# Kernel optimization log

Hardware: AMD Instinct MI355X
Metric: run time of the kernel (lower is better)

The kernel has to match this reference:

```python
import jax, jax.numpy as jnp
import numpy as np

DIM = 1536      # model dim
NH = 12         # num heads
HD = 128        # head dim
F, H, W = 3, 26, 48   # video latent grid (frames, height, width)
S = F * H * W   # sequence length = 3744
B = 1
EPS = 1e-6
C2 = HD // 2    # 64 rotary pairs per head
SPLITS = [C2 - 2 * (C2 // 3), C2 // 3, C2 // 3]  # [22, 21, 21] for (f, h, w)


def _rope_angles():
    """Wan rope_params: concat of per-axis inverse-frequency angle tables, [1024, 64]."""
    def rp(dim):  # returns [1024, dim//2]
        inv = 1.0 / (10000.0 ** (np.arange(0, dim, 2, dtype=np.float64) / dim))
        return np.outer(np.arange(1024, dtype=np.float64), inv)
    a = np.concatenate([rp(HD - 4 * (HD // 6)), rp(2 * (HD // 6)), rp(2 * (HD // 6))], axis=1)
    return jnp.asarray(a, jnp.float32)


def setup_inputs() -> dict:
    key = jax.random.key(0)
    ks = jax.random.split(key, 9)
    std = DIM ** -0.5
    return {
        "x": jax.random.normal(ks[0], (B, S, DIM), jnp.float32),
        "wq": jax.random.normal(ks[1], (DIM, DIM), jnp.float32) * std,
        "bq": jnp.zeros((DIM,), jnp.float32),
        "wk": jax.random.normal(ks[2], (DIM, DIM), jnp.float32) * std,
        "bk": jnp.zeros((DIM,), jnp.float32),
        "wv": jax.random.normal(ks[3], (DIM, DIM), jnp.float32) * std,
        "bv": jnp.zeros((DIM,), jnp.float32),
        "wo": jax.random.normal(ks[4], (DIM, DIM), jnp.float32) * std,
        "bo": jnp.zeros((DIM,), jnp.float32),
        "gq": jnp.ones((DIM,), jnp.float32),   # WanRMSNorm weight for q
        "gk": jnp.ones((DIM,), jnp.float32),   # WanRMSNorm weight for k
        "freqs": _rope_angles(),                # [1024, 64] rotary angles
        "seq_lens": jnp.full((B,), S, jnp.int32),
    }


def _rmsnorm(y, g):
    return y * jax.lax.rsqrt(jnp.mean(jnp.square(y), axis=-1, keepdims=True) + EPS) * g


def _rope_grid(freqs):
    """Build per-position rotary angles [S, C2] from the 3D grid (F,H,W)."""
    af = freqs[:F, :SPLITS[0]]                       # [F, 22]
    ah = freqs[:H, SPLITS[0]:SPLITS[0] + SPLITS[1]]  # [H, 21]
    aw = freqs[:W, SPLITS[0] + SPLITS[1]:]           # [W, 21]
    ang = jnp.concatenate([
        jnp.broadcast_to(af[:, None, None, :], (F, H, W, SPLITS[0])),
        jnp.broadcast_to(ah[None, :, None, :], (F, H, W, SPLITS[1])),
        jnp.broadcast_to(aw[None, None, :, :], (F, H, W, SPLITS[2])),
    ], axis=-1)
    return ang.reshape(S, C2)


def _rope_apply(t, cos, sin):
    # t: [B, S, NH, HD]; pairs (even, odd) rotated by angle.
    tp = t.reshape(B, S, NH, C2, 2)
    xr, xi = tp[..., 0], tp[..., 1]
    yr = xr * cos - xi * sin
    yi = xr * sin + xi * cos
    return jnp.stack([yr, yi], axis=-1).reshape(B, S, NH, HD)


def reference(x, wq, bq, wk, bk, wv, bv, wo, bo, gq, gk, freqs, seq_lens):
    q = _rmsnorm(x @ wq.T + bq, gq).reshape(B, S, NH, HD)
    k = _rmsnorm(x @ wk.T + bk, gk).reshape(B, S, NH, HD)
    v = (x @ wv.T + bv).reshape(B, S, NH, HD)

    ang = _rope_grid(freqs)                    # [S, C2]
    cos = jnp.cos(ang)[None, :, None, :]       # [1, S, 1, C2]
    sin = jnp.sin(ang)[None, :, None, :]
    q = _rope_apply(q, cos, sin)
    k = _rope_apply(k, cos, sin)

    scale = HD ** -0.5
    scores = jnp.einsum('bqhd,bkhd->bhqk', q, k) * scale   # [B, NH, S, S]
    kmask = jnp.arange(S)[None, :] < seq_lens[:, None]     # [B, S]
    scores = jnp.where(kmask[:, None, None, :], scores, jnp.float32(-1e9))
    attn = jax.nn.softmax(scores, axis=-1)
    out = jnp.einsum('bhqk,bkhd->bqhd', attn, v).reshape(B, S, DIM)
    return out @ wo.T + bo
```

## Files before the change

### kernel.cpp

```cpp
#include <hip/hip_runtime.h>
#include <stdint.h>


#define DIM   1536
#define S_TOT 3744
#define NHEAD 12
#define HD    128

using short8 = __attribute__((ext_vector_type(8))) short;
using f32x4  = __attribute__((ext_vector_type(4))) float;
using f32x2  = __attribute__((ext_vector_type(2))) float;

__device__ __forceinline__ unsigned short f2bf(float f) {
  unsigned u = __builtin_bit_cast(unsigned, f);
  u += 0x7fffu + ((u >> 16) & 1u);
  return (unsigned short)(u >> 16);
}

__device__ __forceinline__ void gl_lds16(const void* g, void* l) {
  auto gp = (const __attribute__((address_space(1))) unsigned int*)g;
  auto lp = (__attribute__((address_space(3))) unsigned int*)(uintptr_t)l;
  __builtin_amdgcn_global_load_lds(gp, lp, 16, 0, 0);
}

#define NX4 (S_TOT * DIM / 4)
#define NW4 (DIM * DIM / 4)
__global__ __launch_bounds__(256) void cvt5_kernel(
    const float* __restrict__ x, const float* __restrict__ wq,
    const float* __restrict__ wk, const float* __restrict__ wv,
    const float* __restrict__ wo,
    unsigned short* __restrict__ xb, unsigned short* __restrict__ wqb,
    unsigned short* __restrict__ wkb, unsigned short* __restrict__ wvb,
    unsigned short* __restrict__ wob) {
  int gid = blockIdx.x * 256 + threadIdx.x;
  const float* src; unsigned short* dst; int off;
  if (gid < NX4)                { src = x;  dst = xb;  off = gid; }
  else if (gid < NX4 + NW4)     { src = wq; dst = wqb; off = gid - NX4; }
  else if (gid < NX4 + 2 * NW4) { src = wk; dst = wkb; off = gid - NX4 - NW4; }
  else if (gid < NX4 + 3 * NW4) { src = wv; dst = wvb; off = gid - NX4 - 2 * NW4; }
  else if (gid < NX4 + 4 * NW4) { src = wo; dst = wob; off = gid - NX4 - 3 * NW4; }
  else return;
  float4 v = ((const float4*)src)[off];
  ushort4 o;
  o.x = f2bf(v.x); o.y = f2bf(v.y); o.z = f2bf(v.z); o.w = f2bf(v.w);
  ((ushort4*)dst)[off] = o;
}

__device__ __forceinline__ void gemm_body(const unsigned short* __restrict__ A,
                                          const unsigned short* __restrict__ W,
                                          const float* __restrict__ bias,
                                          float* __restrict__ outF,
                                          unsigned short* __restrict__ outB,
                                          int M, int mode) {
  constexpr int K = DIM, N = DIM;
  __shared__ unsigned short As[128 * 32];
  __shared__ unsigned short Ws[128 * 32];
  int tid = threadIdx.x;
  int w = tid >> 6, lane = tid & 63;
  int wr = w >> 1, wc = w & 1, q4 = lane >> 4, ql = lane & 15;
  int m0 = blockIdx.y * 128, n0 = blockIdx.x * 128;

  f32x4 acc[4][4];
  const f32x4 zero4 = {0.f, 0.f, 0.f, 0.f};
#pragma unroll
  for (int i = 0; i < 4; i++)
#pragma unroll
    for (int j = 0; j < 4; j++) acc[i][j] = zero4;

  for (int k0 = 0; k0 < K; k0 += 32) {
    __syncthreads();
#pragma unroll
    for (int r = 0; r < 2; r++) {
      int idx = r * 256 + tid;
      int row = idx >> 2, ch = idx & 3;
      int am = m0 + row; am = (am < M) ? am : (M - 1);
      gl_lds16(A + (size_t)am * K + k0 + ch * 8, &As[idx * 8]);
      gl_lds16(W + (size_t)(n0 + row) * K + k0 + ch * 8, &Ws[idx * 8]);
    }
    __syncthreads();
    short8 af[4], wf[4];
#pragma unroll
    for (int i = 0; i < 4; i++)
      af[i] = *(const short8*)&As[(wr * 64 + i * 16 + ql) * 32 + q4 * 8];
#pragma unroll
    for (int j = 0; j < 4; j++)
      wf[j] = *(const short8*)&Ws[(wc * 64 + j * 16 + ql) * 32 + q4 * 8];
#pragma unroll
    for (int i = 0; i < 4; i++)
#pragma unroll
      for (int j = 0; j < 4; j++)
        acc[i][j] = __builtin_amdgcn_mfma_f32_16x16x32_bf16(af[i], wf[j], acc[i][j], 0, 0, 0);
  }

  float bb[4];
#pragma unroll
  for (int j = 0; j < 4; j++) bb[j] = bias[n0 + wc * 64 + j * 16 + ql];
#pragma unroll
  for (int i = 0; i < 4; i++) {
#pragma unroll
    for (int rg = 0; rg < 4; rg++) {
      int row = m0 + wr * 64 + i * 16 + q4 * 4 + rg;
      if (row < M) {
#pragma unroll
        for (int j = 0; j < 4; j++) {
          int col = n0 + wc * 64 + j * 16 + ql;
          float v = acc[i][j][rg] + bb[j];
          if (mode == 0) outF[(size_t)row * N + col] = v;
          else           outB[(size_t)row * N + col] = f2bf(v);
        }
      }
    }
  }
}

__global__ __launch_bounds__(256) void gemm_qkv_kernel(
    const unsigned short* __restrict__ xb,
    const unsigned short* __restrict__ wqb, const unsigned short* __restrict__ wkb,
    const unsigned short* __restrict__ wvb,
    const float* __restrict__ bq, const float* __restrict__ bk, const float* __restrict__ bv,
    float* __restrict__ Yq, float* __restrict__ Yk, unsigned short* __restrict__ Vb) {
  int z = blockIdx.z;
  const unsigned short* W = (z == 0) ? wqb : ((z == 1) ? wkb : wvb);
  const float* bias       = (z == 0) ? bq  : ((z == 1) ? bk  : bv);
  float* outF             = (z == 0) ? Yq  : Yk;
  gemm_body(xb, W, bias, outF, Vb, S_TOT, (z == 2) ? 1 : 0);
}

__global__ __launch_bounds__(256) void gemm_out_kernel(
    const unsigned short* __restrict__ AO, const unsigned short* __restrict__ wob,
    const float* __restrict__ bo, float* __restrict__ out) {
  gemm_body(AO, wob, bo, out, nullptr, S_TOT, 0);
}

__global__ __launch_bounds__(256) void normrope_kernel(
    const float* __restrict__ Yq, const float* __restrict__ Yk,
    const float* __restrict__ gq, const float* __restrict__ gk,
    const float* __restrict__ freqs,
    unsigned short* __restrict__ Qb, unsigned short* __restrict__ Kb) {
  int s = blockIdx.x;
  int tid = threadIdx.x;
  int w = tid >> 6, lane = tid & 63;
  const f32x2* yq2 = (const f32x2*)(Yq + (size_t)s * DIM);
  const f32x2* yk2 = (const f32x2*)(Yk + (size_t)s * DIM);
  f32x2 vq[3], vk[3];
  float ssq = 0.f, ssk = 0.f;
#pragma unroll
  for (int r = 0; r < 3; r++) {
    int p = tid + 256 * r;
    vq[r] = yq2[p]; vk[r] = yk2[p];
    ssq += vq[r].x * vq[r].x + vq[r].y * vq[r].y;
    ssk += vk[r].x * vk[r].x + vk[r].y * vk[r].y;
  }
#pragma unroll
  for (int d = 1; d < 64; d <<= 1) {
    ssq += __shfl_xor(ssq, d);
    ssk += __shfl_xor(ssk, d);
  }
  __shared__ float rq[4], rk[4];
  if (lane == 0) { rq[w] = ssq; rk[w] = ssk; }
  __syncthreads();
  float tq = rq[0] + rq[1] + rq[2] + rq[3];
  float tk = rk[0] + rk[1] + rk[2] + rk[3];
  float invq = rsqrtf(tq * (1.f / DIM) + 1e-6f);
  float invk = rsqrtf(tk * (1.f / DIM) + 1e-6f);

  int fi = s / (26 * 48);
  int hi = (s / 48) % 26;
  int wi = s % 48;
#pragma unroll
  for (int r = 0; r < 3; r++) {
    int p = tid + 256 * r;
    int c = p & 63;
    int frow = (c < 22) ? fi : ((c < 43) ? hi : wi);
    float ang = freqs[frow * 64 + c];
    float sn, cs;
    __sincosf(ang, &sn, &cs);
    {
      float a = vq[r].x * invq * gq[2 * p];
      float b = vq[r].y * invq * gq[2 * p + 1];
      ushort2 o; o.x = f2bf(a * cs - b * sn); o.y = f2bf(a * sn + b * cs);
      ((ushort2*)Qb)[(size_t)s * (DIM / 2) + p] = o;
    }
    {
      float a = vk[r].x * invk * gk[2 * p];
      float b = vk[r].y * invk * gk[2 * p + 1];
      ushort2 o; o.x = f2bf(a * cs - b * sn); o.y = f2bf(a * sn + b * cs);
      ((ushort2*)Kb)[(size_t)s * (DIM / 2) + p] = o;
    }
  }
}

__global__ __launch_bounds__(256) void vtrans_kernel(const unsigned short* __restrict__ Vb,
                                                     unsigned short* __restrict__ Vt) {
  int d0 = blockIdx.x * 64, s0 = blockIdx.y * 64;
  __shared__ unsigned short t[64][65];
  int tid = threadIdx.x;
#pragma unroll
  for (int r = 0; r < 4; r++) {
    int idx = r * 256 + tid;
    int sr = idx >> 4, c4 = (idx & 15) * 4;
    ushort4 v; v.x = v.y = v.z = v.w = 0;
    int s = s0 + sr;
    if (s < S_TOT) v = *(const ushort4*)(Vb + (size_t)s * DIM + d0 + c4);
    t[sr][c4 + 0] = v.x; t[sr][c4 + 1] = v.y; t[sr][c4 + 2] = v.z; t[sr][c4 + 3] = v.w;
  }
  __syncthreads();
#pragma unroll
  for (int r = 0; r < 4; r++) {
    int idx = r * 256 + tid;
    int dr = idx >> 4, s4 = (idx & 15) * 4;
    if (s0 + s4 < S_TOT) {
      ushort4 v;
      v.x = t[s4 + 0][dr]; v.y = t[s4 + 1][dr]; v.z = t[s4 + 2][dr]; v.w = t[s4 + 3][dr];
      *(ushort4*)(Vt + (size_t)(d0 + dr) * S_TOT + s0 + s4) = v;
    }
  }
}

__global__ __launch_bounds__(128, 2) void attn_kernel(
    const unsigned short* __restrict__ Qb, const unsigned short* __restrict__ Kb,
    const unsigned short* __restrict__ Vt, unsigned short* __restrict__ AO,
    const int* __restrict__ seq_lens) {
  int h = blockIdx.y;
  int tid = threadIdx.x;
  int w = tid >> 6, lane = tid & 63;
  int q4 = lane >> 4, ql = lane & 15;
  int seqlen = seq_lens[0]; if (seqlen > S_TOT) seqlen = S_TOT;

  __shared__ unsigned short Kl[64 * 128];
  __shared__ unsigned short Vl[128 * 64];
  __shared__ unsigned short Pl[2][32 * 72];
  __shared__ float stat[2][32];

  int q0 = blockIdx.x * 64 + w * 32;
  bool wact = (q0 < S_TOT);

  short8 qf[2][4];
#pragma unroll
  for (int qh = 0; qh < 2; qh++) {
    int qrow = q0 + qh * 16 + ql; if (qrow > S_TOT - 1) qrow = S_TOT - 1;
#pragma unroll
    for (int ks = 0; ks < 4; ks++)
      qf[qh][ks] = *(const short8*)(Qb + (size_t)qrow * DIM + h * HD + ks * 32 + q4 * 8);
  }

  f32x4 o[2][8];
  const f32x4 zero4 = {0.f, 0.f, 0.f, 0.f};
#pragma unroll
  for (int qh = 0; qh < 2; qh++)
#pragma unroll
    for (int nt = 0; nt < 8; nt++) o[qh][nt] = zero4;
  float m_run[2] = {-3.0e38f, -3.0e38f}, l_run[2] = {0.f, 0.f};
  const float sm_scale = 0.08838834764831845f;

  const size_t hoff = (size_t)h * HD;

  for (int kt = 0; kt < (S_TOT + 63) / 64; kt++) {
    int k0 = kt * 64;
    __syncthreads();
    {
      const unsigned short* kseg = Kb + (size_t)k0 * DIM + hoff;
#pragma unroll
      for (int r = 0; r < 8; r++) {
        int idx = r * 128 + tid;
        int row = idx >> 4, c = idx & 15;
        int g = c ^ (row & 15);
        gl_lds16(kseg + (size_t)row * DIM + g * 8, &Kl[idx * 8]);
      }
      int kmax = S_TOT - 8 - k0;
#pragma unroll
      for (int r = 0; r < 8; r++) {
        int idx = r * 128 + tid;
        int row = idx >> 3, c = idx & 7;
        int g = c ^ (row & 7);
        int kc = g * 8; if (kc > kmax) kc = kmax;
        gl_lds16(Vt + (hoff + row) * S_TOT + k0 + kc, &Vl[idx * 8]);
      }
    }
    __syncthreads();
    if (!wact) continue;

    f32x4 st[4][2];
#pragma unroll
    for (int mt = 0; mt < 4; mt++) {
      st[mt][0] = zero4; st[mt][1] = zero4;
#pragma unroll
      for (int ks = 0; ks < 4; ks++) {
        int c = (ks * 4 + q4) ^ ql;
        short8 kf = *(const short8*)&Kl[(mt * 16 + ql) * 128 + c * 8];
        st[mt][0] = __builtin_amdgcn_mfma_f32_16x16x32_bf16(kf, qf[0][ks], st[mt][0], 0, 0, 0);
        st[mt][1] = __builtin_amdgcn_mfma_f32_16x16x32_bf16(kf, qf[1][ks], st[mt][1], 0, 0, 0);
      }
    }

#pragma unroll
    for (int qh = 0; qh < 2; qh++) {
      float sc[16];
      float mloc = -3.0e38f;
#pragma unroll
      for (int mt = 0; mt < 4; mt++)
#pragma unroll
        for (int rg = 0; rg < 4; rg++) {
          int key = k0 + mt * 16 + q4 * 4 + rg;
          float v = st[mt][qh][rg] * sm_scale;
          v = (key < seqlen) ? v : -3.0e38f;
          sc[mt * 4 + rg] = v;
          mloc = fmaxf(mloc, v);
        }
      mloc = fmaxf(mloc, __shfl_xor(mloc, 16));
      mloc = fmaxf(mloc, __shfl_xor(mloc, 32));
      float mnew = fmaxf(m_run[qh], mloc);
      float alpha = __expf(m_run[qh] - mnew);
      m_run[qh] = mnew;
      float lloc = 0.f;
#pragma unroll
      for (int mt = 0; mt < 4; mt++) {
        ushort4 pk;
        float p0 = (k0 + mt * 16 + q4 * 4 + 0 < seqlen) ? __expf(sc[mt * 4 + 0] - mnew) : 0.f;
        float p1 = (k0 + mt * 16 + q4 * 4 + 1 < seqlen) ? __expf(sc[mt * 4 + 1] - mnew) : 0.f;
        float p2 = (k0 + mt * 16 + q4 * 4 + 2 < seqlen) ? __expf(sc[mt * 4 + 2] - mnew) : 0.f;
        float p3 = (k0 + mt * 16 + q4 * 4 + 3 < seqlen) ? __expf(sc[mt * 4 + 3] - mnew) : 0.f;
        lloc += p0 + p1 + p2 + p3;
        pk.x = f2bf(p0); pk.y = f2bf(p1); pk.z = f2bf(p2); pk.w = f2bf(p3);
        *(ushort4*)&Pl[w][(qh * 16 + ql) * 72 + mt * 16 + q4 * 4] = pk;
      }
      lloc += __shfl_xor(lloc, 16);
      lloc += __shfl_xor(lloc, 32);
      l_run[qh] = l_run[qh] * alpha + lloc;
      if (lane < 16) stat[w][qh * 16 + lane] = alpha;
    }

    float ar[2][4];
#pragma unroll
    for (int qh = 0; qh < 2; qh++)
#pragma unroll
      for (int rg = 0; rg < 4; rg++) ar[qh][rg] = stat[w][qh * 16 + q4 * 4 + rg];
#pragma unroll
    for (int qh = 0; qh < 2; qh++)
#pragma unroll
      for (int nt = 0; nt < 8; nt++)
#pragma unroll
        for (int rg = 0; rg < 4; rg++) o[qh][nt][rg] *= ar[qh][rg];

#pragma unroll
    for (int ks2 = 0; ks2 < 2; ks2++) {
      short8 pa0 = *(const short8*)&Pl[w][(0 * 16 + ql) * 72 + ks2 * 32 + q4 * 8];
      short8 pa1 = *(const short8*)&Pl[w][(1 * 16 + ql) * 72 + ks2 * 32 + q4 * 8];
#pragma unroll
      for (int nt = 0; nt < 8; nt++) {
        int c = (ks2 * 4 + q4) ^ (ql & 7);
        short8 vb = *(const short8*)&Vl[(nt * 16 + ql) * 64 + c * 8];
        o[0][nt] = __builtin_amdgcn_mfma_f32_16x16x32_bf16(pa0, vb, o[0][nt], 0, 0, 0);
        o[1][nt] = __builtin_amdgcn_mfma_f32_16x16x32_bf16(pa1, vb, o[1][nt], 0, 0, 0);
      }
    }
  }

  if (wact) {
    if (lane < 16) {
      stat[w][lane]      = 1.0f / l_run[0];
      stat[w][16 + lane] = 1.0f / l_run[1];
    }
#pragma unroll
    for (int qh = 0; qh < 2; qh++) {
#pragma unroll
      for (int rg = 0; rg < 4; rg++) {
        int row = q0 + qh * 16 + q4 * 4 + rg;
        if (row < S_TOT) {
          float il = stat[w][qh * 16 + q4 * 4 + rg];
#pragma unroll
          for (int nt = 0; nt < 8; nt++)
            AO[(size_t)row * DIM + h * HD + nt * 16 + ql] = f2bf(o[qh][nt][rg] * il);
        }
      }
    }
  }
}

extern "C" void kernel_launch(void* const* d_in, const int* in_sizes, int n_in,
                              void* d_out, int out_size, void* d_ws, size_t ws_size,
                              hipStream_t stream) {
  const float* x    = (const float*)d_in[0];
  const float* wq   = (const float*)d_in[1];
  const float* bq   = (const float*)d_in[2];
  const float* wk   = (const float*)d_in[3];
  const float* bk   = (const float*)d_in[4];
  const float* wv   = (const float*)d_in[5];
  const float* bv   = (const float*)d_in[6];
  const float* wo   = (const float*)d_in[7];
  const float* bo   = (const float*)d_in[8];
  const float* gq   = (const float*)d_in[9];
  const float* gk   = (const float*)d_in[10];
  const float* freqs = (const float*)d_in[11];
  const int*   seq  = (const int*)d_in[12];

  char* ws = (char*)d_ws;
  const size_t SZ_X = (size_t)S_TOT * DIM * 2;
  const size_t SZ_W = (size_t)DIM * DIM * 2;
  const size_t SZ_Y = (size_t)S_TOT * DIM * 4;

  unsigned short* xb  = (unsigned short*)(ws);
  unsigned short* wqb = (unsigned short*)(ws + SZ_X);
  unsigned short* wkb = (unsigned short*)(ws + SZ_X + SZ_W);
  unsigned short* wvb = (unsigned short*)(ws + SZ_X + 2 * SZ_W);
  unsigned short* wob = (unsigned short*)(ws + SZ_X + 3 * SZ_W);
  float*          Yq  = (float*)(ws + SZ_X + 4 * SZ_W);
  float*          Yk  = (float*)(ws + SZ_X + 4 * SZ_W + SZ_Y);
  unsigned short* Vb  = (unsigned short*)(ws + SZ_X + 4 * SZ_W + 2 * SZ_Y);
  unsigned short* Qb  = (unsigned short*)(ws + SZ_X + 4 * SZ_W + 2 * SZ_Y + SZ_X);
  unsigned short* Kb  = (unsigned short*)(ws + SZ_X + 4 * SZ_W + 2 * SZ_Y + 2 * SZ_X);
  unsigned short* Vt  = (unsigned short*)(ws + SZ_X + 4 * SZ_W + 2 * SZ_Y + 3 * SZ_X);
  unsigned short* AO  = (unsigned short*)(ws + SZ_X + 4 * SZ_W + 2 * SZ_Y + 4 * SZ_X);

  int total4 = NX4 + 4 * NW4;
  cvt5_kernel<<<dim3((total4 + 255) / 256), 256, 0, stream>>>(
      x, wq, wk, wv, wo, xb, wqb, wkb, wvb, wob);

  gemm_qkv_kernel<<<dim3(DIM / 128, (S_TOT + 127) / 128, 3), 256, 0, stream>>>(
      xb, wqb, wkb, wvb, bq, bk, bv, Yq, Yk, Vb);

  normrope_kernel<<<dim3(S_TOT), 256, 0, stream>>>(Yq, Yk, gq, gk, freqs, Qb, Kb);

  vtrans_kernel<<<dim3(DIM / 64, (S_TOT + 63) / 64), 256, 0, stream>>>(Vb, Vt);

  attn_kernel<<<dim3((S_TOT + 63) / 64, NHEAD), 128, 0, stream>>>(Qb, Kb, Vt, AO, seq);

  gemm_out_kernel<<<dim3(DIM / 128, (S_TOT + 127) / 128), 256, 0, stream>>>(
      AO, wob, bo, (float*)d_out);
}
```

Measured before the change: 473.9 us.

## Split attention into four 16-row waves with lazy rescale and exp2 softmax

```diff
diff --git a/kernel.cpp b/kernel.cpp
--- a/kernel.cpp
+++ b/kernel.cpp
@@ -217,7 +217,7 @@
   }
 }
 
-__global__ __launch_bounds__(128, 2) void attn_kernel(
+__global__ __launch_bounds__(256, 3) void attn_kernel(
     const unsigned short* __restrict__ Qb, const unsigned short* __restrict__ Kb,
     const unsigned short* __restrict__ Vt, unsigned short* __restrict__ AO,
     const int* __restrict__ seq_lens) {
@@ -229,29 +229,25 @@
 
   __shared__ unsigned short Kl[64 * 128];
   __shared__ unsigned short Vl[128 * 64];
-  __shared__ unsigned short Pl[2][32 * 72];
-  __shared__ float stat[2][32];
-
-  int q0 = blockIdx.x * 64 + w * 32;
+  __shared__ unsigned short Pl[4][16 * 72];
+
+  int q0 = blockIdx.x * 64 + w * 16;
   bool wact = (q0 < S_TOT);
 
-  short8 qf[2][4];
-#pragma unroll
-  for (int qh = 0; qh < 2; qh++) {
-    int qrow = q0 + qh * 16 + ql; if (qrow > S_TOT - 1) qrow = S_TOT - 1;
+  short8 qf[4];
+  {
+    int qrow = q0 + ql; if (qrow > S_TOT - 1) qrow = S_TOT - 1;
 #pragma unroll
     for (int ks = 0; ks < 4; ks++)
-      qf[qh][ks] = *(const short8*)(Qb + (size_t)qrow * DIM + h * HD + ks * 32 + q4 * 8);
-  }
-
-  f32x4 o[2][8];
+      qf[ks] = *(const short8*)(Qb + (size_t)qrow * DIM + h * HD + ks * 32 + q4 * 8);
+  }
+
+  f32x4 o[8];
   const f32x4 zero4 = {0.f, 0.f, 0.f, 0.f};
 #pragma unroll
-  for (int qh = 0; qh < 2; qh++)
-#pragma unroll
-    for (int nt = 0; nt < 8; nt++) o[qh][nt] = zero4;
-  float m_run[2] = {-3.0e38f, -3.0e38f}, l_run[2] = {0.f, 0.f};
-  const float sm_scale = 0.08838834764831845f;
+  for (int nt = 0; nt < 8; nt++) o[nt] = zero4;
+  float m_run = -3.0e38f, l_run = 0.f;
+  const float sm_l2 = 0.08838834764831845f * 1.4426950408889634f;
 
   const size_t hoff = (size_t)h * HD;
 
@@ -261,16 +257,16 @@
     {
       const unsigned short* kseg = Kb + (size_t)k0 * DIM + hoff;
 #pragma unroll
-      for (int r = 0; r < 8; r++) {
-        int idx = r * 128 + tid;
+      for (int r = 0; r < 4; r++) {
+        int idx = r * 256 + tid;
         int row = idx >> 4, c = idx & 15;
         int g = c ^ (row & 15);
         gl_lds16(kseg + (size_t)row * DIM + g * 8, &Kl[idx * 8]);
       }
       int kmax = S_TOT - 8 - k0;
 #pragma unroll
-      for (int r = 0; r < 8; r++) {
-        int idx = r * 128 + tid;
+      for (int r = 0; r < 4; r++) {
+        int idx = r * 256 + tid;
         int row = idx >> 3, c = idx & 7;
         int g = c ^ (row & 7);
         int kc = g * 8; if (kc > kmax) kc = kmax;
@@ -280,98 +276,93 @@
     __syncthreads();
     if (!wact) continue;
 
-    f32x4 st[4][2];
+    f32x4 st[4];
 #pragma unroll
     for (int mt = 0; mt < 4; mt++) {
-      st[mt][0] = zero4; st[mt][1] = zero4;
+      st[mt] = zero4;
 #pragma unroll
       for (int ks = 0; ks < 4; ks++) {
         int c = (ks * 4 + q4) ^ ql;
         short8 kf = *(const short8*)&Kl[(mt * 16 + ql) * 128 + c * 8];
-        st[mt][0] = __builtin_amdgcn_mfma_f32_16x16x32_bf16(kf, qf[0][ks], st[mt][0], 0, 0, 0);
-        st[mt][1] = __builtin_amdgcn_mfma_f32_16x16x32_bf16(kf, qf[1][ks], st[mt][1], 0, 0, 0);
-      }
-    }
-
-#pragma unroll
-    for (int qh = 0; qh < 2; qh++) {
-      float sc[16];
-      float mloc = -3.0e38f;
+        st[mt] = __builtin_amdgcn_mfma_f32_16x16x32_bf16(kf, qf[ks], st[mt], 0, 0, 0);
+      }
+    }
+
+    float sc[16];
+#pragma unroll
+    for (int mt = 0; mt < 4; mt++)
+#pragma unroll
+      for (int rg = 0; rg < 4; rg++)
+        sc[mt * 4 + rg] = st[mt][rg] * sm_l2;
+    if (k0 + 64 > seqlen) {
 #pragma unroll
       for (int mt = 0; mt < 4; mt++)
 #pragma unroll
         for (int rg = 0; rg < 4; rg++) {
           int key = k0 + mt * 16 + q4 * 4 + rg;
-          float v = st[mt][qh][rg] * sm_scale;
-          v = (key < seqlen) ? v : -3.0e38f;
-          sc[mt * 4 + rg] = v;
-          mloc = fmaxf(mloc, v);
+          if (key >= seqlen) sc[mt * 4 + rg] = -3.0e38f;
         }
-      mloc = fmaxf(mloc, __shfl_xor(mloc, 16));
-      mloc = fmaxf(mloc, __shfl_xor(mloc, 32));
-      float mnew = fmaxf(m_run[qh], mloc);
-      float alpha = __expf(m_run[qh] - mnew);
-      m_run[qh] = mnew;
-      float lloc = 0.f;
-#pragma unroll
-      for (int mt = 0; mt < 4; mt++) {
-        ushort4 pk;
-        float p0 = (k0 + mt * 16 + q4 * 4 + 0 < seqlen) ? __expf(sc[mt * 4 + 0] - mnew) : 0.f;
-        float p1 = (k0 + mt * 16 + q4 * 4 + 1 < seqlen) ? __expf(sc[mt * 4 + 1] - mnew) : 0.f;
-        float p2 = (k0 + mt * 16 + q4 * 4 + 2 < seqlen) ? __expf(sc[mt * 4 + 2] - mnew) : 0.f;
-        float p3 = (k0 + mt * 16 + q4 * 4 + 3 < seqlen) ? __expf(sc[mt * 4 + 3] - mnew) : 0.f;
-        lloc += p0 + p1 + p2 + p3;
-        pk.x = f2bf(p0); pk.y = f2bf(p1); pk.z = f2bf(p2); pk.w = f2bf(p3);
-        *(ushort4*)&Pl[w][(qh * 16 + ql) * 72 + mt * 16 + q4 * 4] = pk;
-      }
-      lloc += __shfl_xor(lloc, 16);
-      lloc += __shfl_xor(lloc, 32);
-      l_run[qh] = l_run[qh] * alpha + lloc;
-      if (lane < 16) stat[w][qh * 16 + lane] = alpha;
-    }
-
-    float ar[2][4];
-#pragma unroll
-    for (int qh = 0; qh < 2; qh++)
-#pragma unroll
-      for (int rg = 0; rg < 4; rg++) ar[qh][rg] = stat[w][qh * 16 + q4 * 4 + rg];
-#pragma unroll
-    for (int qh = 0; qh < 2; qh++)
+    }
+    float mloc = -3.0e38f;
+#pragma unroll
+    for (int i = 0; i < 16; i++) mloc = fmaxf(mloc, sc[i]);
+    mloc = fmaxf(mloc, __shfl_xor(mloc, 16));
+    mloc = fmaxf(mloc, __shfl_xor(mloc, 32));
+
+    if (!__all(mloc <= m_run + 8.0f)) {
+      float mnew = fmaxf(m_run, mloc);
+      float alpha = exp2f(m_run - mnew);
+      m_run = mnew;
+      l_run *= alpha;
+      float ar[4];
+#pragma unroll
+      for (int rg = 0; rg < 4; rg++) ar[rg] = __shfl(alpha, q4 * 4 + rg, 16);
 #pragma unroll
       for (int nt = 0; nt < 8; nt++)
 #pragma unroll
-        for (int rg = 0; rg < 4; rg++) o[qh][nt][rg] *= ar[qh][rg];
+        for (int rg = 0; rg < 4; rg++) o[nt][rg] *= ar[rg];
+    }
+
+    float lloc = 0.f;
+#pragma unroll
+    for (int mt = 0; mt < 4; mt++) {
+      float p0 = exp2f(sc[mt * 4 + 0] - m_run);
+      float p1 = exp2f(sc[mt * 4 + 1] - m_run);
+      float p2 = exp2f(sc[mt * 4 + 2] - m_run);
+      float p3 = exp2f(sc[mt * 4 + 3] - m_run);
+      lloc += p0 + p1 + p2 + p3;
+      ushort4 pk;
+      pk.x = f2bf(p0); pk.y = f2bf(p1); pk.z = f2bf(p2); pk.w = f2bf(p3);
+      *(ushort4*)&Pl[w][ql * 72 + mt * 16 + q4 * 4] = pk;
+    }
+    lloc += __shfl_xor(lloc, 16);
+    lloc += __shfl_xor(lloc, 32);
+    l_run += lloc;
 
 #pragma unroll
     for (int ks2 = 0; ks2 < 2; ks2++) {
-      short8 pa0 = *(const short8*)&Pl[w][(0 * 16 + ql) * 72 + ks2 * 32 + q4 * 8];
-      short8 pa1 = *(const short8*)&Pl[w][(1 * 16 + ql) * 72 + ks2 * 32 + q4 * 8];
+      short8 pa = *(const short8*)&Pl[w][ql * 72 + ks2 * 32 + q4 * 8];
 #pragma unroll
       for (int nt = 0; nt < 8; nt++) {
         int c = (ks2 * 4 + q4) ^ (ql & 7);
         short8 vb = *(const short8*)&Vl[(nt * 16 + ql) * 64 + c * 8];
-        o[0][nt] = __builtin_amdgcn_mfma_f32_16x16x32_bf16(pa0, vb, o[0][nt], 0, 0, 0);
-        o[1][nt] = __builtin_amdgcn_mfma_f32_16x16x32_bf16(pa1, vb, o[1][nt], 0, 0, 0);
+        o[nt] = __builtin_amdgcn_mfma_f32_16x16x32_bf16(pa, vb, o[nt], 0, 0, 0);
       }
     }
   }
 
   if (wact) {
-    if (lane < 16) {
-      stat[w][lane]      = 1.0f / l_run[0];
-      stat[w][16 + lane] = 1.0f / l_run[1];
-    }
-#pragma unroll
-    for (int qh = 0; qh < 2; qh++) {
-#pragma unroll
-      for (int rg = 0; rg < 4; rg++) {
-        int row = q0 + qh * 16 + q4 * 4 + rg;
-        if (row < S_TOT) {
-          float il = stat[w][qh * 16 + q4 * 4 + rg];
-#pragma unroll
-          for (int nt = 0; nt < 8; nt++)
-            AO[(size_t)row * DIM + h * HD + nt * 16 + ql] = f2bf(o[qh][nt][rg] * il);
-        }
+    float il = 1.0f / l_run;
+    float ilr[4];
+#pragma unroll
+    for (int rg = 0; rg < 4; rg++) ilr[rg] = __shfl(il, q4 * 4 + rg, 16);
+#pragma unroll
+    for (int rg = 0; rg < 4; rg++) {
+      int row = q0 + q4 * 4 + rg;
+      if (row < S_TOT) {
+#pragma unroll
+        for (int nt = 0; nt < 8; nt++)
+          AO[(size_t)row * DIM + h * HD + nt * 16 + ql] = f2bf(o[nt][rg] * ilr[rg]);
       }
     }
   }
@@ -423,7 +414,7 @@
 
   vtrans_kernel<<<dim3(DIM / 64, (S_TOT + 63) / 64), 256, 0, stream>>>(Vb, Vt);
 
-  attn_kernel<<<dim3((S_TOT + 63) / 64, NHEAD), 128, 0, stream>>>(Qb, Kb, Vt, AO, seq);
+  attn_kernel<<<dim3((S_TOT + 63) / 64, NHEAD), 256, 0, stream>>>(Qb, Kb, Vt, AO, seq);
 
   gemm_out_kernel<<<dim3(DIM / 128, (S_TOT + 127) / 128), 256, 0, stream>>>(
       AO, wob, bo, (float*)d_out);
```

Result: faster. 426.8 us (-9.9%).
